# Kernel tuning notes

Measured on AMD Instinct MI355X. Metric: run time of the kernel, lower is better.

## Reference

```python
import jax, jax.numpy as jnp
import numpy as np

D_MODEL = 1024
NHEAD = 16
DHEAD = D_MODEL // NHEAD
DFF = 4096
B, S = 2, 2048
R = 25                # local_attention_radius = 5*5
K = 5                 # rel_pos_max_distance
W = 2 * R + 1         # window width
EPS = 1e-5


def setup_inputs() -> dict:
    key = jax.random.key(0)
    ks = jax.random.split(key, 12)
    s = 0.02
    g = lambda k, shape: jax.random.normal(k, shape, jnp.float32) * s
    return {
        "src": jax.random.normal(ks[0], (B, S, D_MODEL), jnp.float32),
        # attention in/out projections (W stored [out,in], applied x @ W.T + b)
        "wq": g(ks[1], (D_MODEL, D_MODEL)), "bq": jnp.zeros((D_MODEL,), jnp.float32),
        "wk": g(ks[2], (D_MODEL, D_MODEL)), "bk": jnp.zeros((D_MODEL,), jnp.float32),
        "wv": g(ks[3], (D_MODEL, D_MODEL)), "bv": jnp.zeros((D_MODEL,), jnp.float32),
        "wo": g(ks[4], (D_MODEL, D_MODEL)), "bo": jnp.zeros((D_MODEL,), jnp.float32),
        # relative position embeddings, ids clipped to [-K, K] -> 2K+1 rows
        "rel_emb": g(ks[5], (2 * K + 1, DHEAD)),
        # FFN
        "w1": g(ks[6], (DFF, D_MODEL)), "b1": jnp.zeros((DFF,), jnp.float32),
        "w2": g(ks[7], (D_MODEL, DFF)), "b2": jnp.zeros((D_MODEL,), jnp.float32),
        # layernorms
        "g1": jnp.ones((D_MODEL,), jnp.float32), "beta1": jnp.zeros((D_MODEL,), jnp.float32),
        "g2": jnp.ones((D_MODEL,), jnp.float32), "beta2": jnp.zeros((D_MODEL,), jnp.float32),
    }


def _layernorm(x, g, b):
    m = x.mean(-1, keepdims=True)
    v = ((x - m) ** 2).mean(-1, keepdims=True)
    return (x - m) * jax.lax.rsqrt(v + EPS) * g + b


def _rel_window_attention(x, wq, bq, wk, bk, wv, bv, wo, bo, rel_emb):
    b, s, d = x.shape

    def proj(w, bias):
        return (x @ w.T + bias).reshape(b, s, NHEAD, DHEAD).transpose(0, 2, 1, 3)

    q = proj(wq, bq)  # [B,H,S,Dh]
    k = proj(wk, bk)
    v = proj(wv, bv)

    offsets = jnp.arange(-R, R + 1)                     # [W]
    j = jnp.arange(s)[:, None] + offsets[None, :]       # [S,W] absolute key index
    valid = (j >= 0) & (j < s)
    jc = jnp.clip(j, 0, s - 1)

    scale = 1.0 / np.sqrt(DHEAD).astype(np.float32)
    k_win = k[:, :, jc]                                 # [B,H,S,W,Dh] banded gather
    scores = jnp.einsum('bhsd,bhswd->bhsw', q, k_win) * scale
    rel_ids = jnp.clip(offsets, -K, K) + K              # [W]
    scores = scores + jnp.einsum('bhsd,wd->bhsw', q, rel_emb[rel_ids]) * scale
    scores = jnp.where(valid[None, None], scores, jnp.float32(-1e30))
    attn = jax.nn.softmax(scores, axis=-1)              # [B,H,S,W]

    v_win = v[:, :, jc]                                 # [B,H,S,W,Dh]
    out = jnp.einsum('bhsw,bhswd->bhsd', attn, v_win)
    out = out.transpose(0, 2, 1, 3).reshape(b, s, d)
    return out @ wo.T + bo


def reference(src, wq, bq, wk, bk, wv, bv, wo, bo, rel_emb,
              w1, b1, w2, b2, g1, beta1, g2, beta2):
    # post-norm (norm_first=False default) transformer block, dropout=0 (eval)
    z = _rel_window_attention(src, wq, bq, wk, bk, wv, bv, wo, bo, rel_emb)
    x = _layernorm(src + z, g1, beta1)
    ff = jax.nn.relu(x @ w1.T + b1) @ w2.T + b2
    return _layernorm(x + ff, g2, beta2)
```

## Files before the change

kernel.cpp:

```cpp
#include <hip/hip_runtime.h>


#define D_MODEL 1024
#define SEQ     2048
#define NROWS   4096
#define WIN     51
#define RAD     25

typedef __attribute__((ext_vector_type(8))) __bf16 bf16x8;
typedef __attribute__((ext_vector_type(4))) float  floatx4;

__device__ __forceinline__ unsigned short f2bf(float x) {
    unsigned u = __float_as_uint(x);
    unsigned r = u + 0x7fffu + ((u >> 16) & 1u);
    return (unsigned short)(r >> 16);
}
__device__ __forceinline__ float bf2f(unsigned short h) {
    return __uint_as_float(((unsigned)h) << 16);
}

__device__ __forceinline__ void gld16(const unsigned short* g, unsigned short* l) {
    __builtin_amdgcn_global_load_lds(
        (const __attribute__((address_space(1))) unsigned int*)g,
        (__attribute__((address_space(3))) unsigned int*)l,
        16, 0, 0);
}

__device__ __forceinline__ void cvtgrp(const float* __restrict__ in,
                                       unsigned short* __restrict__ out, int g) {
    float4 f = ((const float4*)in)[g];
    ushort4 u;
    u.x = f2bf(f.x); u.y = f2bf(f.y); u.z = f2bf(f.z); u.w = f2bf(f.w);
    ((ushort4*)out)[g] = u;
}

__global__ __launch_bounds__(256)
void cvt_all(const float* __restrict__ src,
             const float* __restrict__ wq, const float* __restrict__ wk,
             const float* __restrict__ wv, const float* __restrict__ wo,
             const float* __restrict__ w1, const float* __restrict__ w2,
             const float* __restrict__ bq, const float* __restrict__ bk,
             const float* __restrict__ bv,
             unsigned short* __restrict__ xb,
             unsigned short* __restrict__ wqkvb,
             unsigned short* __restrict__ wob,
             unsigned short* __restrict__ w1b,
             unsigned short* __restrict__ w2b,
             float* __restrict__ bqkv)
{
    int g = blockIdx.x * 256 + threadIdx.x;
    if (g >= 4194496) return;
    if (g < 1048576) { cvtgrp(src, xb, g); return; }
    g -= 1048576;
    if (g < 262144) { cvtgrp(wq, wqkvb, g); return; }
    g -= 262144;
    if (g < 262144) { cvtgrp(wk, wqkvb + 1048576, g); return; }
    g -= 262144;
    if (g < 262144) { cvtgrp(wv, wqkvb + 2097152, g); return; }
    g -= 262144;
    if (g < 262144) { cvtgrp(wo, wob, g); return; }
    g -= 262144;
    if (g < 1048576) { cvtgrp(w1, w1b, g); return; }
    g -= 1048576;
    if (g < 1048576) { cvtgrp(w2, w2b, g); return; }
    g -= 1048576;
    float4 f = (g < 64) ? ((const float4*)bq)[g]
             : (g < 128) ? ((const float4*)bk)[g - 64]
                         : ((const float4*)bv)[g - 128];
    ((float4*)bqkv)[g] = f;
}

#define BM 128
#define BN 128
#define BK 32

__global__ __launch_bounds__(256, 4)
void gemm_bt(const unsigned short* __restrict__ A,
             const unsigned short* __restrict__ Wt,
             const float* __restrict__ bias,
             unsigned short* __restrict__ Cb,
             int kstride, int kloop, int T, int ldc, int relu)
{
    __shared__ __attribute__((aligned(16))) unsigned short As[2][BM * BK];
    __shared__ __attribute__((aligned(16))) unsigned short Bs[2][BN * BK];

    const int id = blockIdx.x;
    const int s  = id / T;
    const int t  = id - s * T;
    const int sid  = (t & 7) * (T >> 3) + (t >> 3);
    const int rect = sid >> 5;
    const int r    = sid & 31;
    const int bm = ((rect & 7) * 4 + (r >> 3)) * BM;
    const int bn = ((rect >> 3) * 8 + (r & 7)) * BN;

    const int tid  = threadIdx.x;
    const int lane = tid & 63;
    const int wave = tid >> 6;
    const int wm = (wave >> 1) * 64;
    const int wn = (wave & 1) * 64;

    const int srow = lane >> 2;
    const int scol = ((lane & 3) ^ ((lane >> 3) & 3)) * 8;
    const int kofs = s * kloop;
    const unsigned short* Ag = A  + (size_t)(bm + wave * 32 + srow) * kstride + kofs + scol;
    const unsigned short* Wg = Wt + (size_t)(bn + wave * 32 + srow) * kstride + kofs + scol;
    const size_t tstep = (size_t)16 * kstride;
    const int lb = wave * 1024;

    const int fm  = lane & 15;
    const int pg8 = ((lane >> 4) ^ ((fm >> 1) & 3)) * 8;

    floatx4 acc[4][4] = {};
    const int iters = kloop >> 5;

    auto issue = [&](int j, int b) {
        const unsigned short* Aj = Ag + j * BK;
        const unsigned short* Wj = Wg + j * BK;
        gld16(Aj,         &As[b][lb]);
        gld16(Aj + tstep, &As[b][lb + 512]);
        gld16(Wj,         &Bs[b][lb]);
        gld16(Wj + tstep, &Bs[b][lb + 512]);
    };

    issue(0, 0);

    for (int j = 0; j < iters; j++) {
        const int cur = j & 1;
        __syncthreads();
        if (j + 1 < iters) issue(j + 1, cur ^ 1);

        bf16x8 af[4], bf[4];
        #pragma unroll
        for (int ii = 0; ii < 4; ii++)
            af[ii] = *(const bf16x8*)(&As[cur][(wm + ii * 16 + fm) * BK + pg8]);
        #pragma unroll
        for (int jj = 0; jj < 4; jj++)
            bf[jj] = *(const bf16x8*)(&Bs[cur][(wn + jj * 16 + fm) * BK + pg8]);
        #pragma unroll
        for (int ii = 0; ii < 4; ii++)
            #pragma unroll
            for (int jj = 0; jj < 4; jj++)
                acc[ii][jj] = __builtin_amdgcn_mfma_f32_16x16x32_bf16(
                    af[ii], bf[jj], acc[ii][jj], 0, 0, 0);
    }

    unsigned short* Co = Cb + (size_t)s * NROWS * ldc;
    const int r0 = bm + wm + (lane >> 4) * 4;
    const int c0e = bn + wn + (lane & 15);
    #pragma unroll
    for (int i = 0; i < 4; i++) {
        #pragma unroll
        for (int j = 0; j < 4; j++) {
            const int col = c0e + j * 16;
            const float bv = bias ? bias[col] : 0.0f;
            #pragma unroll
            for (int rr = 0; rr < 4; rr++) {
                const int row = r0 + i * 16 + rr;
                float v = acc[i][j][rr] + bv;
                if (relu) v = fmaxf(v, 0.0f);
                Co[(size_t)row * ldc + col] = f2bf(v);
            }
        }
    }
}

#define ROT3(x) ((x) == 16384 ? 0 : (x) + 8192)

__global__ __launch_bounds__(512, 2)
void gemm256(const unsigned short* __restrict__ A,
             const unsigned short* __restrict__ Wt,
             const float* __restrict__ bias,
             unsigned short* __restrict__ Cb,
             int kstride, int kloop, int T, int tncnt,
             int ldc, int relu, size_t sstep1, size_t sstep2)
{
    __shared__ __attribute__((aligned(16))) unsigned short AS[3 * 8192];
    __shared__ __attribute__((aligned(16))) unsigned short BS[3 * 8192];

    const int id = blockIdx.x;
    const int s  = id / T;
    const int t0 = id - s * T;
    const int sid = (t0 & 7) * (T >> 3) + (t0 >> 3);
    const int bm = (sid / tncnt) * 256;
    const int bn = (sid % tncnt) * 256;

    const int tid  = threadIdx.x;
    const int lane = tid & 63;
    const int wave = tid >> 6;
    const int wr   = wave >> 2;
    const int wc   = wave & 3;
    const int fm   = lane & 15;
    const int fq   = lane >> 4;

    const int kofs = s * kloop;
    const int NT   = kloop >> 5;

    const int ks  = (tid >> 3) & 7;
    const int gi  = tid ^ ks;
    const int r0s = gi >> 2;
    const int c2s = gi & 3;
    const unsigned short* Agp = A  + (size_t)(bm + r0s) * kstride + kofs + c2s * 8;
    const unsigned short* Wgp = Wt + (size_t)(bn + r0s) * kstride + kofs + c2s * 8;
    const size_t istep = (size_t)128 * kstride;

    const int rA  = wr * 128 + fm;
    const int rB  = wc * 64  + fm;
    const int c0A = ((((rA << 2) | fq) ^ (fm >> 1)) << 3);
    const int c0B = ((((rB << 2) | fq) ^ (fm >> 1)) << 3);

    gld16(Agp,              AS + tid * 8);
    gld16(Agp + istep,      AS + tid * 8 + 4096);
    gld16(Wgp,              BS + tid * 8);
    gld16(Wgp + istep,      BS + tid * 8 + 4096);
    gld16(Agp + 32,         AS + 8192 + tid * 8);
    gld16(Agp + 32 + istep, AS + 8192 + tid * 8 + 4096);
    gld16(Wgp + 32,         BS + 8192 + tid * 8);
    gld16(Wgp + 32 + istep, BS + 8192 + tid * 8 + 4096);
    asm volatile("s_waitcnt vmcnt(4)" ::: "memory");
    __builtin_amdgcn_sched_barrier(0);
    __builtin_amdgcn_s_barrier();
    __builtin_amdgcn_sched_barrier(0);

    floatx4 acc[8][4] = {};
    const unsigned short* Aga = Agp + 64;
    const unsigned short* Wga = Wgp + 64;
    int cb = 0;
    int pb = 16384;

    for (int t = 0; t < NT; t++) {
        const bool pf = (t + 2 < NT);
        bf16x8 af[8];
        #pragma unroll
        for (int mi = 0; mi < 8; mi++)
            af[mi] = *(const bf16x8*)(AS + cb + c0A + mi * 512);
        #pragma unroll
        for (int ni = 0; ni < 4; ni++) {
            bf16x8 bfr = *(const bf16x8*)(BS + cb + c0B + ni * 512);
            if (pf) {
                if (ni == 0) gld16(Aga,         AS + pb + tid * 8);
                if (ni == 1) gld16(Aga + istep, AS + pb + tid * 8 + 4096);
                if (ni == 2) gld16(Wga,         BS + pb + tid * 8);
                if (ni == 3) gld16(Wga + istep, BS + pb + tid * 8 + 4096);
            }
            __builtin_amdgcn_s_setprio(1);
            #pragma unroll
            for (int mi = 0; mi < 8; mi++)
                acc[mi][ni] = __builtin_amdgcn_mfma_f32_16x16x32_bf16(
                    af[mi], bfr, acc[mi][ni], 0, 0, 0);
            __builtin_amdgcn_s_setprio(0);
        }
        if (t + 1 < NT) {
            if (pf) asm volatile("s_waitcnt vmcnt(4)" ::: "memory");
            else    asm volatile("s_waitcnt vmcnt(0)" ::: "memory");
            __builtin_amdgcn_sched_barrier(0);
            __builtin_amdgcn_s_barrier();
            __builtin_amdgcn_sched_barrier(0);
        }
        cb = ROT3(cb);
        pb = ROT3(pb);
        Aga += 32;
        Wga += 32;
    }

    unsigned short* Co = Cb + (size_t)(s & 1) * sstep1 + (size_t)(s >> 1) * sstep2;
    const int r0  = bm + wr * 128 + fq * 4;
    const int c0e = bn + wc * 64 + fm;
    #pragma unroll
    for (int mi = 0; mi < 8; mi++) {
        #pragma unroll
        for (int ni = 0; ni < 4; ni++) {
            const int col = c0e + ni * 16;
            const float bv = bias ? bias[col] : 0.0f;
            #pragma unroll
            for (int rr = 0; rr < 4; rr++) {
                const int row = r0 + mi * 16 + rr;
                float v = acc[mi][ni][rr] + bv;
                if (relu) v = fmaxf(v, 0.0f);
                Co[(size_t)row * ldc + col] = f2bf(v);
            }
        }
    }
}

__global__ __launch_bounds__(256, 2)
void attn_mfma(const unsigned short* __restrict__ qkv,
               const float* __restrict__ rel,
               unsigned short* __restrict__ attnb)
{
    __shared__ __attribute__((aligned(16))) unsigned short Qs[64 * 72];
    __shared__ __attribute__((aligned(16))) unsigned short Ks[128 * 72];
    __shared__ __attribute__((aligned(16))) unsigned short Vt[64 * 168];
    __shared__ __attribute__((aligned(16))) unsigned short Rs[16 * 72];
    __shared__ __attribute__((aligned(16))) unsigned short Pl[4 * 16 * 104];
    __shared__ float Qrl[4 * 16 * 12];

    const int t   = threadIdx.x;
    const int blk = blockIdx.x;
    const int st  = blk & 31;
    const int h   = (blk >> 5) & 15;
    const int b   = blk >> 9;
    const int s0  = st << 6;
    const int brow0 = b * SEQ;

    const int trow = t >> 3;
    const int tc   = (t & 7) * 8;
    const uint4 z4 = make_uint4(0, 0, 0, 0);

    #pragma unroll
    for (int p = 0; p < 2; p++) {
        int r = trow + p * 32;
        uint4 v = *(const uint4*)(qkv + (size_t)(brow0 + s0 + r) * 3072 + h * 64 + tc);
        *(uint4*)(Qs + r * 72 + tc) = v;
    }
    #pragma unroll
    for (int p = 0; p < 4; p++) {
        int kr = trow + p * 32;
        int ka = s0 - 25 + kr;
        bool in = (ka >= 0) & (ka < SEQ);
        uint4 kv = z4, vv = z4;
        if (in) {
            kv = *(const uint4*)(qkv + (size_t)(brow0 + ka) * 3072 + 1024 + h * 64 + tc);
            vv = *(const uint4*)(qkv + (size_t)(brow0 + ka) * 3072 + 2048 + h * 64 + tc);
        }
        *(uint4*)(Ks + kr * 72 + tc) = kv;
        const unsigned short* e = (const unsigned short*)&vv;
        #pragma unroll
        for (int j = 0; j < 8; j++)
            Vt[(tc + j) * 168 + kr] = e[j];
    }
    if (t < 176) {
        float4 f = ((const float4*)rel)[t];
        int fi = t * 4, rr = fi >> 6, cc = fi & 63;
        ushort4 u;
        u.x = f2bf(f.x); u.y = f2bf(f.y); u.z = f2bf(f.z); u.w = f2bf(f.w);
        *(ushort4*)(Rs + rr * 72 + cc) = u;
    } else {
        int fi = 704 + (t - 176) * 4, rr = fi >> 6, cc = fi & 63;
        *(ushort4*)(Rs + rr * 72 + cc) = make_ushort4(0, 0, 0, 0);
    }
    {
        int n = t * 4, w2 = n >> 8, rem = n & 255, rr = rem >> 4, cc = 80 + (rem & 15);
        *(ushort4*)(Pl + w2 * (16 * 104) + rr * 104 + cc) = make_ushort4(0, 0, 0, 0);
    }
    for (int idx = t; idx < 320; idx += 256) {
        int r = idx / 5, cchunk = idx % 5;
        *(uint4*)(Vt + r * 168 + 128 + cchunk * 8) = z4;
    }
    __syncthreads();

    const int wave = t >> 6;
    const int lane = t & 63;
    const int fm   = lane & 15;
    const int fk8  = (lane >> 4) * 8;
    const int S0w  = s0 + wave * 16;
    unsigned short* Plw = Pl + wave * (16 * 104);
    float* Ql = Qrl + wave * (16 * 12);

    bf16x8 qa0 = *(const bf16x8*)(Qs + (wave * 16 + fm) * 72 + fk8);
    bf16x8 qa1 = *(const bf16x8*)(Qs + (wave * 16 + fm) * 72 + fk8 + 32);

    floatx4 Sc[5];
    #pragma unroll
    for (int nt = 0; nt < 5; nt++) {
        bf16x8 kb0 = *(const bf16x8*)(Ks + (wave * 16 + nt * 16 + fm) * 72 + fk8);
        bf16x8 kb1 = *(const bf16x8*)(Ks + (wave * 16 + nt * 16 + fm) * 72 + fk8 + 32);
        floatx4 acc = {0.f, 0.f, 0.f, 0.f};
        acc = __builtin_amdgcn_mfma_f32_16x16x32_bf16(qa0, kb0, acc, 0, 0, 0);
        acc = __builtin_amdgcn_mfma_f32_16x16x32_bf16(qa1, kb1, acc, 0, 0, 0);
        Sc[nt] = acc;
    }
    {
        bf16x8 rb0 = *(const bf16x8*)(Rs + fm * 72 + fk8);
        bf16x8 rb1 = *(const bf16x8*)(Rs + fm * 72 + fk8 + 32);
        floatx4 qr = {0.f, 0.f, 0.f, 0.f};
        qr = __builtin_amdgcn_mfma_f32_16x16x32_bf16(qa0, rb0, qr, 0, 0, 0);
        qr = __builtin_amdgcn_mfma_f32_16x16x32_bf16(qa1, rb1, qr, 0, 0, 0);
        if (fm < 12) {
            #pragma unroll
            for (int reg = 0; reg < 4; reg++)
                Ql[((lane >> 4) * 4 + reg) * 12 + fm] = qr[reg];
        }
    }

    float inv[4];
    const int iq0 = (lane >> 4) * 4;
    #pragma unroll
    for (int reg = 0; reg < 4; reg++) {
        const int i = iq0 + reg;
        float sc[5];
        float mx = -1e30f;
        #pragma unroll
        for (int nt = 0; nt < 5; nt++) {
            int c   = nt * 16 + fm;
            int off = c - 25 - i;
            int ka  = S0w - 25 + c;
            bool valid = (off >= -RAD) & (off <= RAD) & (ka >= 0) & (ka < SEQ);
            int rid = min(max(off, -5), 5) + 5;
            float v = valid ? (Sc[nt][reg] + Ql[i * 12 + rid]) * 0.125f : -1e30f;
            sc[nt] = v;
            mx = fmaxf(mx, v);
        }
        #pragma unroll
        for (int o = 1; o < 16; o <<= 1) mx = fmaxf(mx, __shfl_xor(mx, o));
        float sum = 0.f;
        #pragma unroll
        for (int nt = 0; nt < 5; nt++) {
            float e = __expf(sc[nt] - mx);
            sum += e;
            Plw[i * 104 + nt * 16 + fm] = f2bf(e);
        }
        #pragma unroll
        for (int o = 1; o < 16; o <<= 1) sum += __shfl_xor(sum, o);
        inv[reg] = 1.0f / sum;
    }

    floatx4 O[4] = {};
    #pragma unroll
    for (int kc = 0; kc < 3; kc++) {
        bf16x8 pa = *(const bf16x8*)(Plw + fm * 104 + fk8 + kc * 32);
        #pragma unroll
        for (int nt = 0; nt < 4; nt++) {
            bf16x8 vb = *(const bf16x8*)(Vt + (nt * 16 + fm) * 168 + wave * 16 + fk8 + kc * 32);
            O[nt] = __builtin_amdgcn_mfma_f32_16x16x32_bf16(pa, vb, O[nt], 0, 0, 0);
        }
    }

    #pragma unroll
    for (int nt = 0; nt < 4; nt++) {
        const int d = nt * 16 + fm;
        #pragma unroll
        for (int reg = 0; reg < 4; reg++) {
            const int i = iq0 + reg;
            attnb[(size_t)(brow0 + S0w + i) * 1024 + h * 64 + d] = f2bf(O[nt][reg] * inv[reg]);
        }
    }
}

__global__ __launch_bounds__(256)
void ln_fuse(const float* __restrict__ resf,
             const unsigned short* __restrict__ resb,
             const unsigned short* __restrict__ p0,
             const unsigned short* __restrict__ p1,
             const unsigned short* __restrict__ p2,
             const unsigned short* __restrict__ p3,
             const float* __restrict__ cbias,
             const float* __restrict__ gamma,
             const float* __restrict__ beta,
             float* __restrict__ outf,
             unsigned short* __restrict__ outb)
{
    const int wave = threadIdx.x >> 6;
    const int lane = threadIdx.x & 63;
    const int row = blockIdx.x * 4 + wave;
    const size_t base = (size_t)row * D_MODEL;

    float x[16];
    float sum = 0.0f, sq = 0.0f;
    #pragma unroll
    for (int i = 0; i < 4; i++) {
        const int c4 = lane + i * 64;
        ushort4 u0 = ((const ushort4*)(p0 + base))[c4];
        ushort4 u1 = ((const ushort4*)(p1 + base))[c4];
        float4 cb = ((const float4*)cbias)[c4];
        float4 va;
        if (resf) {
            va = ((const float4*)(resf + base))[c4];
        } else {
            ushort4 ua = ((const ushort4*)(resb + base))[c4];
            va.x = bf2f(ua.x); va.y = bf2f(ua.y); va.z = bf2f(ua.z); va.w = bf2f(ua.w);
        }
        float e0 = va.x + bf2f(u0.x) + bf2f(u1.x) + cb.x;
        float e1 = va.y + bf2f(u0.y) + bf2f(u1.y) + cb.y;
        float e2 = va.z + bf2f(u0.z) + bf2f(u1.z) + cb.z;
        float e3 = va.w + bf2f(u0.w) + bf2f(u1.w) + cb.w;
        if (p2) {
            ushort4 u2 = ((const ushort4*)(p2 + base))[c4];
            ushort4 u3 = ((const ushort4*)(p3 + base))[c4];
            e0 += bf2f(u2.x) + bf2f(u3.x);
            e1 += bf2f(u2.y) + bf2f(u3.y);
            e2 += bf2f(u2.z) + bf2f(u3.z);
            e3 += bf2f(u2.w) + bf2f(u3.w);
        }
        x[i*4+0] = e0; x[i*4+1] = e1; x[i*4+2] = e2; x[i*4+3] = e3;
        sum += e0 + e1 + e2 + e3;
        sq  += e0*e0 + e1*e1 + e2*e2 + e3*e3;
    }
    #pragma unroll
    for (int off = 32; off > 0; off >>= 1) {
        sum += __shfl_xor(sum, off);
        sq  += __shfl_xor(sq,  off);
    }
    const float mean = sum * (1.0f / 1024.0f);
    const float var  = sq  * (1.0f / 1024.0f) - mean * mean;
    const float rs   = rsqrtf(var + 1e-5f);

    #pragma unroll
    for (int i = 0; i < 4; i++) {
        const int c4 = lane + i * 64;
        float4 g4 = ((const float4*)gamma)[c4];
        float4 b4 = ((const float4*)beta)[c4];
        float4 o;
        o.x = (x[i*4+0] - mean) * rs * g4.x + b4.x;
        o.y = (x[i*4+1] - mean) * rs * g4.y + b4.y;
        o.z = (x[i*4+2] - mean) * rs * g4.z + b4.z;
        o.w = (x[i*4+3] - mean) * rs * g4.w + b4.w;
        if (outf) ((float4*)(outf + base))[c4] = o;
        if (outb) {
            ushort4 u;
            u.x = f2bf(o.x); u.y = f2bf(o.y); u.z = f2bf(o.z); u.w = f2bf(o.w);
            ((ushort4*)(outb + base))[c4] = u;
        }
    }
}

extern "C" void kernel_launch(void* const* d_in, const int* in_sizes, int n_in,
                              void* d_out, int out_size, void* d_ws, size_t ws_size,
                              hipStream_t stream)
{
    const float* src = (const float*)d_in[0];
    const float* wq  = (const float*)d_in[1];
    const float* bq  = (const float*)d_in[2];
    const float* wk  = (const float*)d_in[3];
    const float* bk  = (const float*)d_in[4];
    const float* wv  = (const float*)d_in[5];
    const float* bv  = (const float*)d_in[6];
    const float* wo  = (const float*)d_in[7];
    const float* bo  = (const float*)d_in[8];
    const float* rel = (const float*)d_in[9];
    const float* w1  = (const float*)d_in[10];
    const float* b1  = (const float*)d_in[11];
    const float* w2  = (const float*)d_in[12];
    const float* b2  = (const float*)d_in[13];
    const float* g1  = (const float*)d_in[14];
    const float* be1 = (const float*)d_in[15];
    const float* g2  = (const float*)d_in[16];
    const float* be2 = (const float*)d_in[17];
    float* out = (float*)d_out;

    char* ws = (char*)d_ws;
    const size_t MB = 1048576;
    unsigned short* wqkvb = (unsigned short*)(ws + 0);
    unsigned short* wob   = (unsigned short*)(ws + 6  * MB);
    unsigned short* w1b   = (unsigned short*)(ws + 8  * MB);
    unsigned short* w2b   = (unsigned short*)(ws + 16 * MB);
    float*          bqkv  = (float*)         (ws + 24 * MB);
    unsigned short* xb    = (unsigned short*)(ws + 25 * MB);
    unsigned short* attnb = xb;
    unsigned short* qkvb  = (unsigned short*)(ws + 33 * MB);
    unsigned short* z01   = (unsigned short*)(ws + 33 * MB);
    unsigned short* x1b   = (unsigned short*)(ws + 49 * MB);
    unsigned short* ff1b  = (unsigned short*)(ws + 57 * MB);
    unsigned short* f01   = (unsigned short*)(ws + 0);
    const size_t SL    = (size_t)NROWS * 1024;
    const size_t SOFF2 = (size_t)12 * MB;

    const dim3 blk(256);
    const dim3 blk5(512);
    cvt_all<<<16385, blk, 0, stream>>>(src, wq, wk, wv, wo, w1, w2, bq, bk, bv,
                                       xb, wqkvb, wob, w1b, w2b, bqkv);
    gemm256<<<192, blk5, 0, stream>>>(xb, wqkvb, bqkv, qkvb, 1024, 1024, 192, 12,
                                      3072, 0, 0, 0);
    attn_mfma<<<1024, blk, 0, stream>>>(qkvb, rel, attnb);
    gemm_bt<<<512, blk, 0, stream>>>(attnb, wob, nullptr, z01, 1024, 512, 256, 1024, 0);
    ln_fuse<<<NROWS / 4, blk, 0, stream>>>(src, nullptr, z01, z01 + SL, nullptr, nullptr,
                                           bo, g1, be1, nullptr, x1b);
    gemm256<<<256, blk5, 0, stream>>>(x1b, w1b, b1, ff1b, 1024, 1024, 256, 16,
                                      4096, 1, 0, 0);
    gemm256<<<256, blk5, 0, stream>>>(ff1b, w2b, nullptr, f01, 4096, 1024, 64, 4,
                                      1024, 0, SL, SOFF2);
    ln_fuse<<<NROWS / 4, blk, 0, stream>>>(nullptr, x1b, f01, f01 + SL,
                                           f01 + SOFF2, f01 + SOFF2 + SL,
                                           b2, g2, be2, out, nullptr);
}
```

Baseline: 312.6 us.

## Restructure gemm256 main loop into two half-phases; use it for out-projection

The gemm256 inner loop is split into two halves. Each half loads half of the A fragments, issues half of the global prefetches, hits a workgroup barrier, then runs a 4x4 block of MFMAs at raised priority. This interleaves memory traffic and compute across waves, ping-pong style. The out-projection now uses gemm256 with 4-way split-K instead of the removed gemm_bt kernel, and the LayerNorm kernel sums four partial results. The extra barriers per iteration and the doubled partial-sum traffic are the tradeoff.

New measurement: 312.2 us. No clear change (-0.1%).

```diff
diff --git a/kernel.cpp b/kernel.cpp
--- a/kernel.cpp
+++ b/kernel.cpp
@@ -70,100 +70,6 @@
     ((float4*)bqkv)[g] = f;
 }
 
-#define BM 128
-#define BN 128
-#define BK 32
-
-__global__ __launch_bounds__(256, 4)
-void gemm_bt(const unsigned short* __restrict__ A,
-             const unsigned short* __restrict__ Wt,
-             const float* __restrict__ bias,
-             unsigned short* __restrict__ Cb,
-             int kstride, int kloop, int T, int ldc, int relu)
-{
-    __shared__ __attribute__((aligned(16))) unsigned short As[2][BM * BK];
-    __shared__ __attribute__((aligned(16))) unsigned short Bs[2][BN * BK];
-
-    const int id = blockIdx.x;
-    const int s  = id / T;
-    const int t  = id - s * T;
-    const int sid  = (t & 7) * (T >> 3) + (t >> 3);
-    const int rect = sid >> 5;
-    const int r    = sid & 31;
-    const int bm = ((rect & 7) * 4 + (r >> 3)) * BM;
-    const int bn = ((rect >> 3) * 8 + (r & 7)) * BN;
-
-    const int tid  = threadIdx.x;
-    const int lane = tid & 63;
-    const int wave = tid >> 6;
-    const int wm = (wave >> 1) * 64;
-    const int wn = (wave & 1) * 64;
-
-    const int srow = lane >> 2;
-    const int scol = ((lane & 3) ^ ((lane >> 3) & 3)) * 8;
-    const int kofs = s * kloop;
-    const unsigned short* Ag = A  + (size_t)(bm + wave * 32 + srow) * kstride + kofs + scol;
-    const unsigned short* Wg = Wt + (size_t)(bn + wave * 32 + srow) * kstride + kofs + scol;
-    const size_t tstep = (size_t)16 * kstride;
-    const int lb = wave * 1024;
-
-    const int fm  = lane & 15;
-    const int pg8 = ((lane >> 4) ^ ((fm >> 1) & 3)) * 8;
-
-    floatx4 acc[4][4] = {};
-    const int iters = kloop >> 5;
-
-    auto issue = [&](int j, int b) {
-        const unsigned short* Aj = Ag + j * BK;
-        const unsigned short* Wj = Wg + j * BK;
-        gld16(Aj,         &As[b][lb]);
-        gld16(Aj + tstep, &As[b][lb + 512]);
-        gld16(Wj,         &Bs[b][lb]);
-        gld16(Wj + tstep, &Bs[b][lb + 512]);
-    };
-
-    issue(0, 0);
-
-    for (int j = 0; j < iters; j++) {
-        const int cur = j & 1;
-        __syncthreads();
-        if (j + 1 < iters) issue(j + 1, cur ^ 1);
-
-        bf16x8 af[4], bf[4];
-        #pragma unroll
-        for (int ii = 0; ii < 4; ii++)
-            af[ii] = *(const bf16x8*)(&As[cur][(wm + ii * 16 + fm) * BK + pg8]);
-        #pragma unroll
-        for (int jj = 0; jj < 4; jj++)
-            bf[jj] = *(const bf16x8*)(&Bs[cur][(wn + jj * 16 + fm) * BK + pg8]);
-        #pragma unroll
-        for (int ii = 0; ii < 4; ii++)
-            #pragma unroll
-            for (int jj = 0; jj < 4; jj++)
-                acc[ii][jj] = __builtin_amdgcn_mfma_f32_16x16x32_bf16(
-                    af[ii], bf[jj], acc[ii][jj], 0, 0, 0);
-    }
-
-    unsigned short* Co = Cb + (size_t)s * NROWS * ldc;
-    const int r0 = bm + wm + (lane >> 4) * 4;
-    const int c0e = bn + wn + (lane & 15);
-    #pragma unroll
-    for (int i = 0; i < 4; i++) {
-        #pragma unroll
-        for (int j = 0; j < 4; j++) {
-            const int col = c0e + j * 16;
-            const float bv = bias ? bias[col] : 0.0f;
-            #pragma unroll
-            for (int rr = 0; rr < 4; rr++) {
-                const int row = r0 + i * 16 + rr;
-                float v = acc[i][j][rr] + bv;
-                if (relu) v = fmaxf(v, 0.0f);
-                Co[(size_t)row * ldc + col] = f2bf(v);
-            }
-        }
-    }
-}
-
 #define ROT3(x) ((x) == 16384 ? 0 : (x) + 8192)
 
 __global__ __launch_bounds__(512, 2)
@@ -229,26 +135,53 @@
 
     for (int t = 0; t < NT; t++) {
         const bool pf = (t + 2 < NT);
-        bf16x8 af[8];
-        #pragma unroll
-        for (int mi = 0; mi < 8; mi++)
-            af[mi] = *(const bf16x8*)(AS + cb + c0A + mi * 512);
-        #pragma unroll
-        for (int ni = 0; ni < 4; ni++) {
-            bf16x8 bfr = *(const bf16x8*)(BS + cb + c0B + ni * 512);
-            if (pf) {
-                if (ni == 0) gld16(Aga,         AS + pb + tid * 8);
-                if (ni == 1) gld16(Aga + istep, AS + pb + tid * 8 + 4096);
-                if (ni == 2) gld16(Wga,         BS + pb + tid * 8);
-                if (ni == 3) gld16(Wga + istep, BS + pb + tid * 8 + 4096);
-            }
-            __builtin_amdgcn_s_setprio(1);
+
+        bf16x8 af0[4], bfr[4];
+        #pragma unroll
+        for (int mi = 0; mi < 4; mi++)
+            af0[mi] = *(const bf16x8*)(AS + cb + c0A + mi * 512);
+        #pragma unroll
+        for (int ni = 0; ni < 4; ni++)
+            bfr[ni] = *(const bf16x8*)(BS + cb + c0B + ni * 512);
+        if (pf) {
+            gld16(Aga,         AS + pb + tid * 8);
+            gld16(Aga + istep, AS + pb + tid * 8 + 4096);
+        }
+        __builtin_amdgcn_sched_barrier(0);
+        __builtin_amdgcn_s_barrier();
+        __builtin_amdgcn_sched_barrier(0);
+        __builtin_amdgcn_s_setprio(1);
+        #pragma unroll
+        for (int mi = 0; mi < 4; mi++)
             #pragma unroll
-            for (int mi = 0; mi < 8; mi++)
+            for (int ni = 0; ni < 4; ni++)
                 acc[mi][ni] = __builtin_amdgcn_mfma_f32_16x16x32_bf16(
-                    af[mi], bfr, acc[mi][ni], 0, 0, 0);
-            __builtin_amdgcn_s_setprio(0);
-        }
+                    af0[mi], bfr[ni], acc[mi][ni], 0, 0, 0);
+        __builtin_amdgcn_s_setprio(0);
+        __builtin_amdgcn_sched_barrier(0);
+        __builtin_amdgcn_s_barrier();
+        __builtin_amdgcn_sched_barrier(0);
+
+        bf16x8 af1[4];
+        #pragma unroll
+        for (int mi = 0; mi < 4; mi++)
+            af1[mi] = *(const bf16x8*)(AS + cb + c0A + (mi + 4) * 512);
+        if (pf) {
+            gld16(Wga,         BS + pb + tid * 8);
+            gld16(Wga + istep, BS + pb + tid * 8 + 4096);
+        }
+        __builtin_amdgcn_sched_barrier(0);
+        __builtin_amdgcn_s_barrier();
+        __builtin_amdgcn_sched_barrier(0);
+        __builtin_amdgcn_s_setprio(1);
+        #pragma unroll
+        for (int mi = 0; mi < 4; mi++)
+            #pragma unroll
+            for (int ni = 0; ni < 4; ni++)
+                acc[mi + 4][ni] = __builtin_amdgcn_mfma_f32_16x16x32_bf16(
+                    af1[mi], bfr[ni], acc[mi + 4][ni], 0, 0, 0);
+        __builtin_amdgcn_s_setprio(0);
+
         if (t + 1 < NT) {
             if (pf) asm volatile("s_waitcnt vmcnt(4)" ::: "memory");
             else    asm volatile("s_waitcnt vmcnt(0)" ::: "memory");
@@ -561,8 +494,10 @@
     gemm256<<<192, blk5, 0, stream>>>(xb, wqkvb, bqkv, qkvb, 1024, 1024, 192, 12,
                                       3072, 0, 0, 0);
     attn_mfma<<<1024, blk, 0, stream>>>(qkvb, rel, attnb);
-    gemm_bt<<<512, blk, 0, stream>>>(attnb, wob, nullptr, z01, 1024, 512, 256, 1024, 0);
-    ln_fuse<<<NROWS / 4, blk, 0, stream>>>(src, nullptr, z01, z01 + SL, nullptr, nullptr,
+    gemm256<<<256, blk5, 0, stream>>>(attnb, wob, nullptr, z01, 1024, 256, 64, 4,
+                                      1024, 0, SL, SOFF2);
+    ln_fuse<<<NROWS / 4, blk, 0, stream>>>(src, nullptr, z01, z01 + SL,
+                                           z01 + SOFF2, z01 + SOFF2 + SL,
                                            bo, g1, be1, nullptr, x1b);
     gemm256<<<256, blk5, 0, stream>>>(x1b, w1b, b1, ff1b, 1024, 1024, 256, 16,
                                       4096, 1, 0, 0);
```
